# Kernel optimization log

Measured on AMD Instinct MI355X. Metric: run time of the kernel, lower is better.

Reference implementation:

```python
import jax, jax.numpy as jnp
import numpy as np

B, T, MEL, C, NL, NSTATE, NFREQ = 16, 1024, 80, 512, 6, 32, 513

def _layer_norm(x, g, b, eps=1e-5):
    mu = x.mean(-1, keepdims=True)
    var = ((x - mu) ** 2).mean(-1, keepdims=True)
    return (x - mu) * jax.lax.rsqrt(var + eps) * g + b

def _s4d(h, logA, Cp, Dp):
    # h: [B,T,C]; diagonal S4D: K[c,t] = sum_n Cp[c,n] * exp(-exp(logA[c,n]) * t)
    t = jnp.arange(T, dtype=h.dtype)
    A = -jnp.exp(logA)                                   # [C,N]
    expA = jnp.exp(A[:, :, None] * t)                    # [C,N,T] Vandermonde
    K = jnp.einsum('cn,cnt->tc', Cp, expA)               # [T,C]
    n_fft = 2 * T
    Xf = jnp.fft.rfft(h, n=n_fft, axis=1)                # [B,F,C]
    Kf = jnp.fft.rfft(K, n=n_fft, axis=0)                # [F,C]
    y = jnp.fft.irfft(Xf * Kf[None], n=n_fft, axis=1)[:, :T, :]
    return jax.nn.gelu(y + Dp * h)

def setup_inputs() -> dict:
    key = jax.random.key(0)
    ks = jax.random.split(key, 16)
    f32 = jnp.float32
    inp = {
        'mel': jax.random.normal(ks[0], (B, T, MEL), f32),
        'w_in': jax.random.normal(ks[1], (MEL, C), f32) * (MEL ** -0.5),
        'b_in': jnp.zeros((C,), f32),
        'freq_emb': jax.random.normal(ks[2], (NFREQ, C), f32) * 0.02,
        's4_logA': jnp.log(0.5 * jnp.ones((NL, C, NSTATE), f32))
                   + 0.1 * jax.random.normal(ks[3], (NL, C, NSTATE), f32),
        's4_C': jax.random.normal(ks[4], (NL, C, NSTATE), f32) * (NSTATE ** -0.5),
        's4_D': jax.random.normal(ks[5], (NL, 1, 1, C), f32),
        'ln_g': jnp.ones((6, C), f32),
        'ln_b': jnp.zeros((6, C), f32),
        'w5': jax.random.normal(ks[6], (5, C), f32) * (C ** -0.5),
        'b5': jnp.zeros((5,), f32),
        'wm': jax.random.normal(ks[7], (C, 13), f32) * (C ** -0.5),
        'bm': jnp.zeros((13,), f32),
    }
    return inp

def reference(mel, w_in, b_in, freq_emb, s4_logA, s4_C, s4_D, ln_g, ln_b, w5, b5, wm, bm):
    x = mel @ w_in + b_in                                # [B,T,C]
    # pad/truncate freq positional embedding along time to T
    if NFREQ >= T:
        freq = freq_emb[:T]
    else:
        pad = jnp.broadcast_to(freq_emb[-1:], (T - NFREQ, C))
        freq = jnp.concatenate([freq_emb, pad], axis=0)
    h = x + freq[None]                                   # [B,T,C]
    for l in range(NL):
        h = _s4d(h, s4_logA[l], s4_C[l], s4_D[l])
    hm = h.mean(axis=1)                                  # [B,C]
    f0        = (_layer_norm(h,  ln_g[0], ln_b[0]) @ w5[0] + b5[0])        # [B,T]
    energy    = (_layer_norm(h,  ln_g[1], ln_b[1]) @ w5[1] + b5[1])        # [B,T]
    pitch_var = (_layer_norm(h,  ln_g[2], ln_b[2]) @ w5[2] + b5[2])        # [B,T]
    speech_rate = (_layer_norm(hm, ln_g[3], ln_b[3]) @ w5[3] + b5[3])[:, None]  # [B,1]
    pause_dur   = (_layer_norm(hm, ln_g[4], ln_b[4]) @ w5[4] + b5[4])[:, None]  # [B,1]
    mfcc        = _layer_norm(hm, ln_g[5], ln_b[5]) @ wm + bm              # [B,13]
    return (f0, energy, pitch_var, speech_rate, pause_dur, mfcc)
```

## Files before the change

kernel.cpp:

```cpp
#include <hip/hip_runtime.h>
#include <hip/hip_bf16.h>

#define B_ 16
#define T_ 1024
#define MEL_ 80
#define C_ 512
#define NL_ 6
#define NS_ 32
#define HBSTR 1096

typedef _Float16 f16x8 __attribute__((ext_vector_type(8)));
typedef float f32x4 __attribute__((ext_vector_type(4)));

__device__ __forceinline__ float wred(float v) {
#pragma unroll
    for (int m = 32; m >= 1; m >>= 1) v += __shfl_xor(v, m, 64);
    return v;
}

__device__ __forceinline__ unsigned int pkh(float a, float b) {
    typedef __fp16 h2 __attribute__((ext_vector_type(2)));
    h2 r = __builtin_amdgcn_cvt_pkrtz(a, b);
    return __builtin_bit_cast(unsigned int, r);
}
__device__ __forceinline__ float h2f(unsigned short u) {
    return (float)__builtin_bit_cast(_Float16, u);
}

__global__ __launch_bounds__(256) void tap_frags(const float* __restrict__ logA,
                                                 const float* __restrict__ Cp,
                                                 const float* __restrict__ Dp,
                                                 unsigned short* __restrict__ AH,
                                                 unsigned short* __restrict__ AL) {
    __shared__ float KT[4][32];
    const int gid0 = blockIdx.x * 4;
    const int tid = threadIdx.x;
    if (tid < 128) {
        int gl = tid >> 5, tau = tid & 31;
        int gid = gid0 + gl;
        const float* la = logA + (size_t)gid * NS_;
        const float* cp = Cp + (size_t)gid * NS_;
        float s = 0.f;
        float t = (float)tau;
#pragma unroll 8
        for (int n = 0; n < NS_; ++n)
            s += cp[n] * expf(-expf(la[n]) * t);
        if (tau == 0) s += Dp[gid];
        KT[gl][tau] = s;
    }
    __syncthreads();
    const int wv = tid >> 6, lane = tid & 63;
    const int gid = gid0 + wv;
    float kv = KT[wv][lane & 31];
    const int m = lane & 15, hh = lane >> 4;
    f16x8 vh, vl;
#pragma unroll
    for (int e = 0; e < 8; ++e) {
        int th = 32 + m - 8 * hh - e;
        int tl = m - 8 * hh - e;
        float a = __shfl(kv, th & 31, 64);
        float bq = __shfl(kv, tl & 31, 64);
        vh[e] = (th >= 0 && th < 32) ? (_Float16)a : (_Float16)0.f;
        vl[e] = (tl >= 0 && tl < 32) ? (_Float16)bq : (_Float16)0.f;
    }
    *(f16x8*)(AH + (size_t)gid * 512 + lane * 8) = vh;
    *(f16x8*)(AL + (size_t)gid * 512 + lane * 8) = vl;
}

__global__ __launch_bounds__(256) void in_proj(const float* __restrict__ mel,
                                               const float* __restrict__ w_in,
                                               const float* __restrict__ b_in,
                                               const float* __restrict__ freq,
                                               float* __restrict__ h0T) {
    const int wid = blockIdx.x * 4 + (threadIdx.x >> 6);
    const int lane = threadIdx.x & 63;
    const int mtile = wid >> 1;
    const int chalf = wid & 1;
    const int rbase = mtile * 16;
    const int b = rbase >> 10;
    const int tloc = rbase & 1023;
    const int n = lane & 15, hh = lane >> 4;

    f16x8 Am[3];
#pragma unroll
    for (int ch = 0; ch < 3; ++ch) {
        f16x8 a = {0, 0, 0, 0, 0, 0, 0, 0};
        if (ch < 2 || hh < 2) {
            const float* mp = mel + (size_t)(rbase + n) * MEL_ + 32 * ch + 8 * hh;
            float4 m0 = *(const float4*)(mp);
            float4 m1 = *(const float4*)(mp + 4);
            a[0] = (_Float16)m0.x; a[1] = (_Float16)m0.y;
            a[2] = (_Float16)m0.z; a[3] = (_Float16)m0.w;
            a[4] = (_Float16)m1.x; a[5] = (_Float16)m1.y;
            a[6] = (_Float16)m1.z; a[7] = (_Float16)m1.w;
        }
        Am[ch] = a;
    }

#pragma unroll 4
    for (int it = 0; it < 16; ++it) {
        const int ct = chalf * 256 + it * 16;
        const int c = ct + n;
        f16x8 Bw[3];
#pragma unroll
        for (int ch = 0; ch < 3; ++ch) {
            f16x8 w = {0, 0, 0, 0, 0, 0, 0, 0};
            if (ch < 2 || hh < 2) {
#pragma unroll
                for (int e = 0; e < 8; ++e)
                    w[e] = (_Float16)w_in[(size_t)(32 * ch + 8 * hh + e) * C_ + c];
            }
            Bw[ch] = w;
        }
        f32x4 d = {0.f, 0.f, 0.f, 0.f};
        d = __builtin_amdgcn_mfma_f32_16x16x32_f16(Am[0], Bw[0], d, 0, 0, 0);
        d = __builtin_amdgcn_mfma_f32_16x16x32_f16(Am[1], Bw[1], d, 0, 0, 0);
        d = __builtin_amdgcn_mfma_f32_16x16x32_f16(Am[2], Bw[2], d, 0, 0, 0);
        float bias = b_in[c];
        float4 v;
#pragma unroll
        for (int r = 0; r < 4; ++r) {
            int t = tloc + 4 * hh + r;
            int fr = t < 513 ? t : 512;
            ((float*)&v)[r] = d[r] + bias + freq[(size_t)fr * C_ + c];
        }
        *(float4*)(h0T + ((size_t)b * C_ + c) * T_ + tloc + 4 * hh) = v;
    }
}

__global__ __launch_bounds__(512) void conv_stack(const float* __restrict__ h0T,
                                                  float* __restrict__ hfin,
                                                  const unsigned short* __restrict__ AH,
                                                  const unsigned short* __restrict__ AL,
                                                  float* __restrict__ hm) {
    __shared__ unsigned short HB[8 * HBSTR];
    const int b = blockIdx.y;
    const int gx = blockIdx.x;
    const int c0 = 8 * (((gx & 7) << 3) | (gx >> 3));
    const int tid = threadIdx.x;
    const int lane = tid & 63;
    const int wv = tid >> 6;
    const int c = __builtin_amdgcn_readfirstlane(c0 + wv);
    unsigned short* hb = &HB[wv * HBSTR];

    if (lane < 32) hb[lane] = 0;
    if (lane < 40) hb[1056 + lane] = 0;

    {
        const float* srcT = h0T + ((size_t)b * C_ + c) * T_ + 16 * lane;
        float4 e0 = *(const float4*)(srcT);
        float4 e1 = *(const float4*)(srcT + 4);
        float4 e2 = *(const float4*)(srcT + 8);
        float4 e3 = *(const float4*)(srcT + 12);
        uint4 p0, p1;
        p0.x = pkh(e0.x, e0.y); p0.y = pkh(e0.z, e0.w);
        p0.z = pkh(e1.x, e1.y); p0.w = pkh(e1.z, e1.w);
        p1.x = pkh(e2.x, e2.y); p1.y = pkh(e2.z, e2.w);
        p1.z = pkh(e3.x, e3.y); p1.w = pkh(e3.z, e3.w);
        *(uint4*)(&hb[32 + 16 * lane]) = p0;
        *(uint4*)(&hb[32 + 16 * lane + 8]) = p1;
    }

    const int n = lane & 15, hh = lane >> 4;
    const int boff = 16 * n + 8 * hh;
    const int woff = 32 + 16 * n + 4 * hh;

    f16x8 Ah = *(const f16x8*)(AH + (size_t)c * 512 + lane * 8);
    f16x8 Al = *(const f16x8*)(AL + (size_t)c * 512 + lane * 8);

    float hsum = 0.f;
    for (int l = 0; l < NL_; ++l) {
        const int ln = (l + 1 < NL_) ? l + 1 : 0;
        f16x8 nAh = *(const f16x8*)(AH + ((size_t)ln * C_ + c) * 512 + lane * 8);
        f16x8 nAl = *(const f16x8*)(AL + ((size_t)ln * C_ + c) * 512 + lane * 8);

        f32x4 d[4];
#pragma unroll
        for (int q = 0; q < 4; ++q) {
            const unsigned short* base = hb + 256 * q + boff;
            f16x8 Bh = *(const f16x8*)(base);
            f16x8 Bl = *(const f16x8*)(base + 32);
            f32x4 z = {0.f, 0.f, 0.f, 0.f};
            d[q] = __builtin_amdgcn_mfma_f32_16x16x32_f16(Ah, Bh, z, 0, 0, 0);
            d[q] = __builtin_amdgcn_mfma_f32_16x16x32_f16(Al, Bl, d[q], 0, 0, 0);
        }
#pragma unroll
        for (int q = 0; q < 4; ++q) {
            float g[4];
#pragma unroll
            for (int r = 0; r < 4; ++r) {
                float y = d[q][r];
                float u2 = y * (y * y * 0.07135481627f + 1.59576912161f);
                float rr = __builtin_amdgcn_rcpf(__expf(u2) + 1.f);
                g[r] = y - y * rr;
            }
            if (l == NL_ - 1) hsum += g[0] + g[1] + g[2] + g[3];
            uint2 pw;
            pw.x = pkh(g[0], g[1]);
            pw.y = pkh(g[2], g[3]);
            *(uint2*)(&hb[woff + 256 * q]) = pw;
        }
        Ah = nAh; Al = nAl;
    }

    {
        float s = wred(hsum);
        if (lane == 0) hm[(size_t)b * C_ + c] = s * (1.f / T_);
    }

    __syncthreads();
    {
        float* dst = hfin + (size_t)b * T_ * C_ + c0;
#pragma unroll
        for (int it = 0; it < 4; ++it) {
            int idx = it * 512 + tid;
            int t = idx >> 1, u = idx & 1;
            float4 v;
            v.x = h2f(HB[(4 * u + 0) * HBSTR + 32 + t]);
            v.y = h2f(HB[(4 * u + 1) * HBSTR + 32 + t]);
            v.z = h2f(HB[(4 * u + 2) * HBSTR + 32 + t]);
            v.w = h2f(HB[(4 * u + 3) * HBSTR + 32 + t]);
            *(float4*)(dst + (size_t)t * C_ + 4 * u) = v;
        }
    }
}

__global__ __launch_bounds__(256) void heads_rows(const float* __restrict__ h,
                                                  const float* __restrict__ ln_g,
                                                  const float* __restrict__ ln_b,
                                                  const float* __restrict__ w5,
                                                  const float* __restrict__ b5,
                                                  float* __restrict__ out) {
    int wv = threadIdx.x >> 6, lane = threadIdx.x & 63;
    int r0 = blockIdx.x * 16 + wv * 4;
    float g[3][8], bb[3][8], ww[3][8];
#pragma unroll
    for (int o = 0; o < 3; ++o) {
        const float* gp = ln_g + o * C_ + lane * 8;
        const float* bp = ln_b + o * C_ + lane * 8;
        const float* wp = w5 + o * C_ + lane * 8;
        float4 a, bq;
        a = *(const float4*)(gp); bq = *(const float4*)(gp + 4);
        g[o][0]=a.x; g[o][1]=a.y; g[o][2]=a.z; g[o][3]=a.w;
        g[o][4]=bq.x; g[o][5]=bq.y; g[o][6]=bq.z; g[o][7]=bq.w;
        a = *(const float4*)(bp); bq = *(const float4*)(bp + 4);
        bb[o][0]=a.x; bb[o][1]=a.y; bb[o][2]=a.z; bb[o][3]=a.w;
        bb[o][4]=bq.x; bb[o][5]=bq.y; bb[o][6]=bq.z; bb[o][7]=bq.w;
        a = *(const float4*)(wp); bq = *(const float4*)(wp + 4);
        ww[o][0]=a.x; ww[o][1]=a.y; ww[o][2]=a.z; ww[o][3]=a.w;
        ww[o][4]=bq.x; ww[o][5]=bq.y; ww[o][6]=bq.z; ww[o][7]=bq.w;
    }
    float b5r[3] = {b5[0], b5[1], b5[2]};
#pragma unroll
    for (int rr = 0; rr < 4; ++rr) {
        const int r = r0 + rr;
        const float* row = h + (size_t)r * C_ + lane * 8;
        float x[8];
        {
            float4 xa = *(const float4*)(row);
            float4 xb = *(const float4*)(row + 4);
            x[0]=xa.x; x[1]=xa.y; x[2]=xa.z; x[3]=xa.w;
            x[4]=xb.x; x[5]=xb.y; x[6]=xb.z; x[7]=xb.w;
        }
        float s = 0.f;
#pragma unroll
        for (int i = 0; i < 8; ++i) s += x[i];
        float mu = wred(s) * (1.f / C_);
        float v = 0.f;
#pragma unroll
        for (int i = 0; i < 8; ++i) { float d = x[i] - mu; v += d * d; }
        float rstd = rsqrtf(wred(v) * (1.f / C_) + 1e-5f);
#pragma unroll
        for (int o = 0; o < 3; ++o) {
            float acc = 0.f;
#pragma unroll
            for (int i = 0; i < 8; ++i) {
                float xn = (x[i] - mu) * rstd * g[o][i] + bb[o][i];
                acc += xn * ww[o][i];
            }
            acc = wred(acc);
            if (lane == 0) out[o * (B_ * T_) + r] = acc + b5r[o];
        }
    }
}

__global__ __launch_bounds__(64) void heads_utt(const float* __restrict__ hm,
                                                const float* __restrict__ ln_g,
                                                const float* __restrict__ ln_b,
                                                const float* __restrict__ w5,
                                                const float* __restrict__ b5,
                                                const float* __restrict__ wm,
                                                const float* __restrict__ bm,
                                                float* __restrict__ out) {
    int b = blockIdx.x;
    int lane = threadIdx.x;
    const float* row = hm + (size_t)b * C_;
    float x[8];
#pragma unroll
    for (int i = 0; i < 8; ++i) x[i] = row[lane + 64 * i];
    float s = 0.f;
#pragma unroll
    for (int i = 0; i < 8; ++i) s += x[i];
    float mu = wred(s) * (1.f / C_);
    float v = 0.f;
#pragma unroll
    for (int i = 0; i < 8; ++i) { float d = x[i] - mu; v += d * d; }
    float rstd = rsqrtf(wred(v) * (1.f / C_) + 1e-5f);

    const int OUT_SR = 3 * B_ * T_;
    const int OUT_PD = OUT_SR + B_;
    const int OUT_MF = OUT_PD + B_;
#pragma unroll
    for (int o = 3; o <= 4; ++o) {
        float acc = 0.f;
#pragma unroll
        for (int i = 0; i < 8; ++i) {
            int cc = lane + 64 * i;
            float xn = (x[i] - mu) * rstd * ln_g[o * C_ + cc] + ln_b[o * C_ + cc];
            acc += xn * w5[o * C_ + cc];
        }
        acc = wred(acc);
        if (lane == 0) out[(o == 3 ? OUT_SR : OUT_PD) + b] = acc + b5[o];
    }
    float mf[13];
#pragma unroll
    for (int j = 0; j < 13; ++j) mf[j] = 0.f;
#pragma unroll
    for (int i = 0; i < 8; ++i) {
        int cc = lane + 64 * i;
        float xn = (x[i] - mu) * rstd * ln_g[5 * C_ + cc] + ln_b[5 * C_ + cc];
#pragma unroll
        for (int j = 0; j < 13; ++j) mf[j] += xn * wm[cc * 13 + j];
    }
#pragma unroll
    for (int j = 0; j < 13; ++j) {
        float m = wred(mf[j]);
        if (lane == 0) out[OUT_MF + b * 13 + j] = m + bm[j];
    }
}

extern "C" void kernel_launch(void* const* d_in, const int* in_sizes, int n_in,
                              void* d_out, int out_size, void* d_ws, size_t ws_size,
                              hipStream_t stream) {
    const float* mel   = (const float*)d_in[0];
    const float* w_in  = (const float*)d_in[1];
    const float* b_in  = (const float*)d_in[2];
    const float* freq  = (const float*)d_in[3];
    const float* logA  = (const float*)d_in[4];
    const float* s4C   = (const float*)d_in[5];
    const float* s4D   = (const float*)d_in[6];
    const float* ln_g  = (const float*)d_in[7];
    const float* ln_b  = (const float*)d_in[8];
    const float* w5    = (const float*)d_in[9];
    const float* b5    = (const float*)d_in[10];
    const float* wm    = (const float*)d_in[11];
    const float* bm    = (const float*)d_in[12];
    float* out = (float*)d_out;

    char* ws = (char*)d_ws;
    const size_t HBYTES = (size_t)B_ * T_ * C_ * sizeof(float);
    float* hA = (float*)ws;
    float* hB = (float*)(ws + HBYTES);
    float* hm = (float*)(ws + 2 * HBYTES);
    unsigned short* AH = (unsigned short*)(ws + 2 * HBYTES +
                                           (size_t)B_ * C_ * sizeof(float));
    unsigned short* AL = AH + (size_t)NL_ * C_ * 512;

    tap_frags<<<(NL_ * C_) / 4, 256, 0, stream>>>(logA, s4C, s4D, AH, AL);
    in_proj<<<512, 256, 0, stream>>>(mel, w_in, b_in, freq, hA);
    conv_stack<<<dim3(C_ / 8, B_), 512, 0, stream>>>(hA, hB, AH, AL, hm);
    heads_rows<<<(B_ * T_) / 16, 256, 0, stream>>>(hB, ln_g, ln_b, w5, b5, out);
    heads_utt<<<B_, 64, 0, stream>>>(hm, ln_g, ln_b, w5, b5, wm, bm, out);
}
```

Baseline: 154.0 us.

## Merge projection and tap kernels; split conv stack across two waves per channel

Folds the input projection and the S4 tap-fragment generation into one launch, with the block index range selecting the role, so one kernel launch is saved. The conv stack kernel now uses 1024 threads with two waves per channel, each handling half the time tiles. It double-buffers the LDS history and adds a block barrier per layer so each wave sees the other half's outputs. The mean reduction now combines two partial sums through shared memory. This doubles per-block parallelism and latency hiding at the cost of per-layer barriers and twice the LDS footprint.

```diff
diff --git a/kernel.cpp b/kernel.cpp
--- a/kernel.cpp
+++ b/kernel.cpp
@@ -27,139 +27,140 @@
     return (float)__builtin_bit_cast(_Float16, u);
 }
 
-__global__ __launch_bounds__(256) void tap_frags(const float* __restrict__ logA,
+__global__ __launch_bounds__(256) void proj_taps(const float* __restrict__ mel,
+                                                 const float* __restrict__ w_in,
+                                                 const float* __restrict__ b_in,
+                                                 const float* __restrict__ freq,
+                                                 const float* __restrict__ logA,
                                                  const float* __restrict__ Cp,
                                                  const float* __restrict__ Dp,
+                                                 float* __restrict__ h0T,
                                                  unsigned short* __restrict__ AH,
                                                  unsigned short* __restrict__ AL) {
     __shared__ float KT[4][32];
-    const int gid0 = blockIdx.x * 4;
-    const int tid = threadIdx.x;
-    if (tid < 128) {
-        int gl = tid >> 5, tau = tid & 31;
-        int gid = gid0 + gl;
-        const float* la = logA + (size_t)gid * NS_;
-        const float* cp = Cp + (size_t)gid * NS_;
-        float s = 0.f;
-        float t = (float)tau;
+    if (blockIdx.x < 512) {
+        const int wid = blockIdx.x * 4 + (threadIdx.x >> 6);
+        const int lane = threadIdx.x & 63;
+        const int mtile = wid >> 1;
+        const int chalf = wid & 1;
+        const int rbase = mtile * 16;
+        const int b = rbase >> 10;
+        const int tloc = rbase & 1023;
+        const int n = lane & 15, hh = lane >> 4;
+
+        f16x8 Am[3];
+#pragma unroll
+        for (int ch = 0; ch < 3; ++ch) {
+            f16x8 a = {0, 0, 0, 0, 0, 0, 0, 0};
+            if (ch < 2 || hh < 2) {
+                const float* mp = mel + (size_t)(rbase + n) * MEL_ + 32 * ch + 8 * hh;
+                float4 m0 = *(const float4*)(mp);
+                float4 m1 = *(const float4*)(mp + 4);
+                a[0] = (_Float16)m0.x; a[1] = (_Float16)m0.y;
+                a[2] = (_Float16)m0.z; a[3] = (_Float16)m0.w;
+                a[4] = (_Float16)m1.x; a[5] = (_Float16)m1.y;
+                a[6] = (_Float16)m1.z; a[7] = (_Float16)m1.w;
+            }
+            Am[ch] = a;
+        }
+#pragma unroll 4
+        for (int it = 0; it < 16; ++it) {
+            const int ct = chalf * 256 + it * 16;
+            const int c = ct + n;
+            f16x8 Bw[3];
+#pragma unroll
+            for (int ch = 0; ch < 3; ++ch) {
+                f16x8 w = {0, 0, 0, 0, 0, 0, 0, 0};
+                if (ch < 2 || hh < 2) {
+#pragma unroll
+                    for (int e = 0; e < 8; ++e)
+                        w[e] = (_Float16)w_in[(size_t)(32 * ch + 8 * hh + e) * C_ + c];
+                }
+                Bw[ch] = w;
+            }
+            f32x4 d = {0.f, 0.f, 0.f, 0.f};
+            d = __builtin_amdgcn_mfma_f32_16x16x32_f16(Am[0], Bw[0], d, 0, 0, 0);
+            d = __builtin_amdgcn_mfma_f32_16x16x32_f16(Am[1], Bw[1], d, 0, 0, 0);
+            d = __builtin_amdgcn_mfma_f32_16x16x32_f16(Am[2], Bw[2], d, 0, 0, 0);
+            float bias = b_in[c];
+            float4 v;
+#pragma unroll
+            for (int r = 0; r < 4; ++r) {
+                int t = tloc + 4 * hh + r;
+                int fr = t < 513 ? t : 512;
+                ((float*)&v)[r] = d[r] + bias + freq[(size_t)fr * C_ + c];
+            }
+            *(float4*)(h0T + ((size_t)b * C_ + c) * T_ + tloc + 4 * hh) = v;
+        }
+    } else {
+        const int gid0 = (blockIdx.x - 512) * 4;
+        const int tid = threadIdx.x;
+        if (tid < 128) {
+            int gl = tid >> 5, tau = tid & 31;
+            int gid = gid0 + gl;
+            const float* la = logA + (size_t)gid * NS_;
+            const float* cp = Cp + (size_t)gid * NS_;
+            float s = 0.f;
+            float t = (float)tau;
 #pragma unroll 8
-        for (int n = 0; n < NS_; ++n)
-            s += cp[n] * expf(-expf(la[n]) * t);
-        if (tau == 0) s += Dp[gid];
-        KT[gl][tau] = s;
-    }
-    __syncthreads();
-    const int wv = tid >> 6, lane = tid & 63;
-    const int gid = gid0 + wv;
-    float kv = KT[wv][lane & 31];
-    const int m = lane & 15, hh = lane >> 4;
-    f16x8 vh, vl;
-#pragma unroll
-    for (int e = 0; e < 8; ++e) {
-        int th = 32 + m - 8 * hh - e;
-        int tl = m - 8 * hh - e;
-        float a = __shfl(kv, th & 31, 64);
-        float bq = __shfl(kv, tl & 31, 64);
-        vh[e] = (th >= 0 && th < 32) ? (_Float16)a : (_Float16)0.f;
-        vl[e] = (tl >= 0 && tl < 32) ? (_Float16)bq : (_Float16)0.f;
-    }
-    *(f16x8*)(AH + (size_t)gid * 512 + lane * 8) = vh;
-    *(f16x8*)(AL + (size_t)gid * 512 + lane * 8) = vl;
-}
-
-__global__ __launch_bounds__(256) void in_proj(const float* __restrict__ mel,
-                                               const float* __restrict__ w_in,
-                                               const float* __restrict__ b_in,
-                                               const float* __restrict__ freq,
-                                               float* __restrict__ h0T) {
-    const int wid = blockIdx.x * 4 + (threadIdx.x >> 6);
-    const int lane = threadIdx.x & 63;
-    const int mtile = wid >> 1;
-    const int chalf = wid & 1;
-    const int rbase = mtile * 16;
-    const int b = rbase >> 10;
-    const int tloc = rbase & 1023;
-    const int n = lane & 15, hh = lane >> 4;
-
-    f16x8 Am[3];
-#pragma unroll
-    for (int ch = 0; ch < 3; ++ch) {
-        f16x8 a = {0, 0, 0, 0, 0, 0, 0, 0};
-        if (ch < 2 || hh < 2) {
-            const float* mp = mel + (size_t)(rbase + n) * MEL_ + 32 * ch + 8 * hh;
-            float4 m0 = *(const float4*)(mp);
-            float4 m1 = *(const float4*)(mp + 4);
-            a[0] = (_Float16)m0.x; a[1] = (_Float16)m0.y;
-            a[2] = (_Float16)m0.z; a[3] = (_Float16)m0.w;
-            a[4] = (_Float16)m1.x; a[5] = (_Float16)m1.y;
-            a[6] = (_Float16)m1.z; a[7] = (_Float16)m1.w;
-        }
-        Am[ch] = a;
-    }
-
-#pragma unroll 4
-    for (int it = 0; it < 16; ++it) {
-        const int ct = chalf * 256 + it * 16;
-        const int c = ct + n;
-        f16x8 Bw[3];
-#pragma unroll
-        for (int ch = 0; ch < 3; ++ch) {
-            f16x8 w = {0, 0, 0, 0, 0, 0, 0, 0};
-            if (ch < 2 || hh < 2) {
-#pragma unroll
-                for (int e = 0; e < 8; ++e)
-                    w[e] = (_Float16)w_in[(size_t)(32 * ch + 8 * hh + e) * C_ + c];
-            }
-            Bw[ch] = w;
-        }
-        f32x4 d = {0.f, 0.f, 0.f, 0.f};
-        d = __builtin_amdgcn_mfma_f32_16x16x32_f16(Am[0], Bw[0], d, 0, 0, 0);
-        d = __builtin_amdgcn_mfma_f32_16x16x32_f16(Am[1], Bw[1], d, 0, 0, 0);
-        d = __builtin_amdgcn_mfma_f32_16x16x32_f16(Am[2], Bw[2], d, 0, 0, 0);
-        float bias = b_in[c];
-        float4 v;
-#pragma unroll
-        for (int r = 0; r < 4; ++r) {
-            int t = tloc + 4 * hh + r;
-            int fr = t < 513 ? t : 512;
-            ((float*)&v)[r] = d[r] + bias + freq[(size_t)fr * C_ + c];
-        }
-        *(float4*)(h0T + ((size_t)b * C_ + c) * T_ + tloc + 4 * hh) = v;
-    }
-}
-
-__global__ __launch_bounds__(512) void conv_stack(const float* __restrict__ h0T,
-                                                  float* __restrict__ hfin,
-                                                  const unsigned short* __restrict__ AH,
-                                                  const unsigned short* __restrict__ AL,
-                                                  float* __restrict__ hm) {
-    __shared__ unsigned short HB[8 * HBSTR];
+            for (int nn = 0; nn < NS_; ++nn)
+                s += cp[nn] * expf(-expf(la[nn]) * t);
+            if (tau == 0) s += Dp[gid];
+            KT[gl][tau] = s;
+        }
+        __syncthreads();
+        const int wv = tid >> 6, lane = tid & 63;
+        const int gid = gid0 + wv;
+        float kv = KT[wv][lane & 31];
+        const int m = lane & 15, hh = lane >> 4;
+        f16x8 vh, vl;
+#pragma unroll
+        for (int e = 0; e < 8; ++e) {
+            int th = 32 + m - 8 * hh - e;
+            int tl = m - 8 * hh - e;
+            float a = __shfl(kv, th & 31, 64);
+            float bq = __shfl(kv, tl & 31, 64);
+            vh[e] = (th >= 0 && th < 32) ? (_Float16)a : (_Float16)0.f;
+            vl[e] = (tl >= 0 && tl < 32) ? (_Float16)bq : (_Float16)0.f;
+        }
+        *(f16x8*)(AH + (size_t)gid * 512 + lane * 8) = vh;
+        *(f16x8*)(AL + (size_t)gid * 512 + lane * 8) = vl;
+    }
+}
+
+__global__ __launch_bounds__(1024) void conv_stack(const float* __restrict__ h0T,
+                                                   float* __restrict__ hfin,
+                                                   const unsigned short* __restrict__ AH,
+                                                   const unsigned short* __restrict__ AL,
+                                                   float* __restrict__ hm) {
+    __shared__ unsigned short HB[2][8 * HBSTR];
+    __shared__ float HS[16];
     const int b = blockIdx.y;
     const int gx = blockIdx.x;
     const int c0 = 8 * (((gx & 7) << 3) | (gx >> 3));
     const int tid = threadIdx.x;
     const int lane = tid & 63;
     const int wv = tid >> 6;
-    const int c = __builtin_amdgcn_readfirstlane(c0 + wv);
-    unsigned short* hb = &HB[wv * HBSTR];
-
-    if (lane < 32) hb[lane] = 0;
-    if (lane < 40) hb[1056 + lane] = 0;
+    const int ch = wv >> 1;
+    const int half = wv & 1;
+    const int c = __builtin_amdgcn_readfirstlane(c0 + ch);
+
+    unsigned short* hb0 = &HB[0][ch * HBSTR];
+    unsigned short* hb1 = &HB[1][ch * HBSTR];
+
+    if (half == 0 && lane < 32) { hb0[lane] = 0; hb1[lane] = 0; }
+    if (half == 1 && lane < 40) { hb0[1056 + lane] = 0; hb1[1056 + lane] = 0; }
 
     {
-        const float* srcT = h0T + ((size_t)b * C_ + c) * T_ + 16 * lane;
-        float4 e0 = *(const float4*)(srcT);
-        float4 e1 = *(const float4*)(srcT + 4);
-        float4 e2 = *(const float4*)(srcT + 8);
-        float4 e3 = *(const float4*)(srcT + 12);
-        uint4 p0, p1;
-        p0.x = pkh(e0.x, e0.y); p0.y = pkh(e0.z, e0.w);
-        p0.z = pkh(e1.x, e1.y); p0.w = pkh(e1.z, e1.w);
-        p1.x = pkh(e2.x, e2.y); p1.y = pkh(e2.z, e2.w);
-        p1.z = pkh(e3.x, e3.y); p1.w = pkh(e3.z, e3.w);
-        *(uint4*)(&hb[32 + 16 * lane]) = p0;
-        *(uint4*)(&hb[32 + 16 * lane + 8]) = p1;
-    }
+        const float* src = h0T + ((size_t)b * C_ + c) * T_ + 512 * half + 8 * lane;
+        float4 e0 = *(const float4*)(src);
+        float4 e1 = *(const float4*)(src + 4);
+        uint4 p;
+        p.x = pkh(e0.x, e0.y); p.y = pkh(e0.z, e0.w);
+        p.z = pkh(e1.x, e1.y); p.w = pkh(e1.z, e1.w);
+        *(uint4*)(&hb0[32 + 512 * half + 8 * lane]) = p;
+    }
+    __syncthreads();
 
     const int n = lane & 15, hh = lane >> 4;
     const int boff = 16 * n + 8 * hh;
@@ -170,26 +171,30 @@
 
     float hsum = 0.f;
     for (int l = 0; l < NL_; ++l) {
+        const unsigned short* cur = (l & 1) ? hb1 : hb0;
+        unsigned short* nxt = (l & 1) ? hb0 : hb1;
         const int ln = (l + 1 < NL_) ? l + 1 : 0;
         f16x8 nAh = *(const f16x8*)(AH + ((size_t)ln * C_ + c) * 512 + lane * 8);
         f16x8 nAl = *(const f16x8*)(AL + ((size_t)ln * C_ + c) * 512 + lane * 8);
 
-        f32x4 d[4];
-#pragma unroll
-        for (int q = 0; q < 4; ++q) {
-            const unsigned short* base = hb + 256 * q + boff;
+        f32x4 d[2];
+#pragma unroll
+        for (int qq = 0; qq < 2; ++qq) {
+            const int q = 2 * half + qq;
+            const unsigned short* base = cur + 256 * q + boff;
             f16x8 Bh = *(const f16x8*)(base);
             f16x8 Bl = *(const f16x8*)(base + 32);
             f32x4 z = {0.f, 0.f, 0.f, 0.f};
-            d[q] = __builtin_amdgcn_mfma_f32_16x16x32_f16(Ah, Bh, z, 0, 0, 0);
-            d[q] = __builtin_amdgcn_mfma_f32_16x16x32_f16(Al, Bl, d[q], 0, 0, 0);
-        }
-#pragma unroll
-        for (int q = 0; q < 4; ++q) {
+            d[qq] = __builtin_amdgcn_mfma_f32_16x16x32_f16(Ah, Bh, z, 0, 0, 0);
+            d[qq] = __builtin_amdgcn_mfma_f32_16x16x32_f16(Al, Bl, d[qq], 0, 0, 0);
+        }
+#pragma unroll
+        for (int qq = 0; qq < 2; ++qq) {
+            const int q = 2 * half + qq;
             float g[4];
 #pragma unroll
             for (int r = 0; r < 4; ++r) {
-                float y = d[q][r];
+                float y = d[qq][r];
                 float u2 = y * (y * y * 0.07135481627f + 1.59576912161f);
                 float rr = __builtin_amdgcn_rcpf(__expf(u2) + 1.f);
                 g[r] = y - y * rr;
@@ -198,28 +203,31 @@
             uint2 pw;
             pw.x = pkh(g[0], g[1]);
             pw.y = pkh(g[2], g[3]);
-            *(uint2*)(&hb[woff + 256 * q]) = pw;
+            *(uint2*)(&nxt[woff + 256 * q]) = pw;
         }
         Ah = nAh; Al = nAl;
+        __syncthreads();
     }
 
     {
         float s = wred(hsum);
-        if (lane == 0) hm[(size_t)b * C_ + c] = s * (1.f / T_);
-    }
-
+        if (lane == 0) HS[wv] = s;
+    }
     __syncthreads();
+    if (tid < 8)
+        hm[(size_t)b * C_ + c0 + tid] = (HS[2 * tid] + HS[2 * tid + 1]) * (1.f / T_);
+
     {
         float* dst = hfin + (size_t)b * T_ * C_ + c0;
 #pragma unroll
-        for (int it = 0; it < 4; ++it) {
-            int idx = it * 512 + tid;
+        for (int it = 0; it < 2; ++it) {
+            int idx = it * 1024 + tid;
             int t = idx >> 1, u = idx & 1;
             float4 v;
-            v.x = h2f(HB[(4 * u + 0) * HBSTR + 32 + t]);
-            v.y = h2f(HB[(4 * u + 1) * HBSTR + 32 + t]);
-            v.z = h2f(HB[(4 * u + 2) * HBSTR + 32 + t]);
-            v.w = h2f(HB[(4 * u + 3) * HBSTR + 32 + t]);
+            v.x = h2f(HB[0][(4 * u + 0) * HBSTR + 32 + t]);
+            v.y = h2f(HB[0][(4 * u + 1) * HBSTR + 32 + t]);
+            v.z = h2f(HB[0][(4 * u + 2) * HBSTR + 32 + t]);
+            v.w = h2f(HB[0][(4 * u + 3) * HBSTR + 32 + t]);
             *(float4*)(dst + (size_t)t * C_ + 4 * u) = v;
         }
     }
@@ -366,9 +374,9 @@
                                            (size_t)B_ * C_ * sizeof(float));
     unsigned short* AL = AH + (size_t)NL_ * C_ * 512;
 
-    tap_frags<<<(NL_ * C_) / 4, 256, 0, stream>>>(logA, s4C, s4D, AH, AL);
-    in_proj<<<512, 256, 0, stream>>>(mel, w_in, b_in, freq, hA);
-    conv_stack<<<dim3(C_ / 8, B_), 512, 0, stream>>>(hA, hB, AH, AL, hm);
+    proj_taps<<<1280, 256, 0, stream>>>(mel, w_in, b_in, freq,
+                                        logA, s4C, s4D, hA, AH, AL);
+    conv_stack<<<dim3(C_ / 8, B_), 1024, 0, stream>>>(hA, hB, AH, AL, hm);
     heads_rows<<<(B_ * T_) / 16, 256, 0, stream>>>(hB, ln_g, ln_b, w5, b5, out);
     heads_utt<<<B_, 64, 0, stream>>>(hm, ln_g, ln_b, w5, b5, wm, bm, out);
 }
```

Result: slower. 159.4 us (+3.6%).
